# Kernel tuning notes

Measured on AMD Instinct MI355X. Metric: run time of the kernel, lower is better.

The kernel has to match this reference:

```python
import jax, jax.numpy as jnp
from jax import lax
import numpy as np

L = 8            # NMF rank (n_components)
NMF_ITERS = 50   # fixed multiplicative-update iterations
EPS = 1.1920929e-07  # float32 machine eps, as sklearn uses


def nmf_mu(V, key):
    """Multiplicative-update NMF (Frobenius loss), sklearn-style random init.
    V: [T, M] nonnegative. Returns W:[T,L], H:[L,M]."""
    T, M = V.shape
    kW, kH = jax.random.split(key)
    avg = jnp.sqrt(jnp.mean(V) / L)
    W0 = avg * jax.random.uniform(kW, (T, L), dtype=V.dtype)
    H0 = avg * jax.random.uniform(kH, (L, M), dtype=V.dtype)

    def step(carry, _):
        W, H = carry
        # H update: H *= (W^T V) / (W^T W H)
        H = H * (W.T @ V) / (W.T @ W @ H + EPS)
        # W update: W *= (V H^T) / (W H H^T)
        W = W * (V @ H.T) / (W @ (H @ H.T) + EPS)
        return (W, H), None

    (W, H), _ = lax.scan(step, (W0, H0), None, length=NMF_ITERS)
    return W, H


def pointwise_conv(w, x):
    # 1x1x1 Conv3d == channel mix: w [C_out, C_in], x [n, C_in, D, H, W]
    return jnp.einsum('oc,ncdhw->nodhw', w, x)


def setup_inputs() -> dict:
    key = jax.random.key(0)
    k0, k1, k2, k3, k4 = jax.random.split(key, 5)
    C = 64
    eps = jax.random.normal(k0, (1, C, 16, 64, 64), dtype=jnp.float32)
    s = 1.0 / np.sqrt(C)  # keep pre-activation variance ~1 (like torch init scale)
    w_pre = jax.random.normal(k1, (C, C), dtype=jnp.float32) * s
    b_pre = jax.random.normal(k2, (C,), dtype=jnp.float32) * s
    w_post1 = jax.random.normal(k3, (C, C), dtype=jnp.float32) * s
    w_post2 = jax.random.normal(k4, (C, C), dtype=jnp.float32) * s
    return {"eps": eps, "w_pre": w_pre, "b_pre": b_pre,
            "w_post1": w_post1, "w_post2": w_post2}


def reference(eps, w_pre, b_pre, w_post1, w_post2):
    n, t, k, a, b = eps.shape
    # xi_pre: 1x1x1 conv + bias + ReLU (ReLU guarantees nonnegative NMF input)
    Vst = jax.nn.relu(pointwise_conv(w_pre, eps) + b_pre[None, :, None, None, None])
    V = Vst.reshape(t, k * a * b)  # n == 1
    W, H = nmf_mu(V, jax.random.key(0))
    Vst_hat = (W @ H).reshape(n, t, k, a, b)
    error = jnp.linalg.norm(Vst - Vst_hat)  # torch.dist (Frobenius)
    # xi_post: conv(no bias) -> ReLU -> conv(no bias)
    y = jax.nn.relu(pointwise_conv(w_post1, Vst_hat))
    eps_hat = pointwise_conv(w_post2, y)
    return eps_hat, error
```

## Files before the change

kernel.cpp:

```cpp
#include <hip/hip_runtime.h>
#include <stdint.h>

#define JAX_PARTITIONABLE 1

constexpr int kC = 64;
constexpr int kS = 65536;
constexpr int kL = 8;
constexpr int kIters = 50;
constexpr int kBlocks = 256;
constexpr int kThreads = 512;
constexpr int kCols = 256;
constexpr int kGroups = 16;
constexpr int kEntries = 576;
constexpr float kEps = 1.1920929e-07f;

#define AGENT __HIP_MEMORY_SCOPE_AGENT

struct Ctl {
  unsigned root;  unsigned pad0[31];
  unsigned leaf[16][32];
  float mean_sum; float err_sum; float pad1[30];
  float B[3][kGroups][kEntries];
};

__device__ __forceinline__ uint2 tf2x32(unsigned k0, unsigned k1,
                                        unsigned x0, unsigned x1) {
  unsigned k2 = k0 ^ k1 ^ 0x1BD11BDAu;
  x0 += k0; x1 += k1;
#define TF_RND(r) { x0 += x1; x1 = (x1 << (r)) | (x1 >> (32 - (r))); x1 ^= x0; }
  TF_RND(13) TF_RND(15) TF_RND(26) TF_RND(6)
  x0 += k1; x1 += k2 + 1u;
  TF_RND(17) TF_RND(29) TF_RND(16) TF_RND(24)
  x0 += k2; x1 += k0 + 2u;
  TF_RND(13) TF_RND(15) TF_RND(26) TF_RND(6)
  x0 += k0; x1 += k1 + 3u;
  TF_RND(17) TF_RND(29) TF_RND(16) TF_RND(24)
  x0 += k1; x1 += k2 + 4u;
  TF_RND(13) TF_RND(15) TF_RND(26) TF_RND(6)
  x0 += k2; x1 += k0 + 5u;
#undef TF_RND
  return make_uint2(x0, x1);
}

__device__ __forceinline__ float u01(unsigned b) {
  return __uint_as_float((b >> 9) | 0x3f800000u) - 1.0f;
}

__device__ __forceinline__ void gridbar(Ctl* ctl, unsigned& round) {
  ++round;
  __syncthreads();
  if (threadIdx.x == 0) {
    const unsigned target = round * 16u;
    const unsigned leaf = blockIdx.x & 15u;
    unsigned a = __hip_atomic_fetch_add(&ctl->leaf[leaf][0], 1u,
                                        __ATOMIC_RELAXED, AGENT);
    if (a == target - 1u)
      __hip_atomic_fetch_add(&ctl->root, 1u, __ATOMIC_RELAXED, AGENT);
    while (__hip_atomic_load(&ctl->root, __ATOMIC_RELAXED, AGENT) < target)
      __builtin_amdgcn_s_sleep(1);
    __builtin_amdgcn_fence(__ATOMIC_ACQUIRE, "agent");
  }
  __syncthreads();
}

__global__ void init_ctl(unsigned* ws) {
  const unsigned n = (unsigned)(sizeof(Ctl) / 4);
  for (unsigned i = blockIdx.x * blockDim.x + threadIdx.x; i < n;
       i += gridDim.x * blockDim.x)
    ws[i] = 0u;
}

__global__ __launch_bounds__(kThreads, 2) void fsam_nmf(
    const float* __restrict__ eps, const float* __restrict__ w_pre,
    const float* __restrict__ b_pre, const float* __restrict__ w_post1,
    const float* __restrict__ w_post2, float* __restrict__ out, Ctl* ctl) {
  __shared__ __align__(16) float Vs[kC][260];
  __shared__ __align__(16) float Hs[kL][260];
  __shared__ __align__(16) float Pn[kL][260];
  __shared__ __align__(16) float Pv[4][512];
  __shared__ __align__(16) float Ph[16][64];
  __shared__ __align__(16) float Ws[kC][kL];
  __shared__ __align__(16) float WtWs[kL * kL];
  __shared__ __align__(16) float hhts[kL * kL];
  __shared__ float reds[8];

  const int tid = threadIdx.x;
  const int t = tid & 255;
  const int q = tid >> 8;
  const int obase = q * 32;
  const int s = blockIdx.x * kCols + t;
  unsigned bar_round = 0;

  float acc[32];
#pragma unroll
  for (int o = 0; o < 32; ++o) acc[o] = b_pre[obase + o];
  for (int c = 0; c < kC; ++c) {
    const float e = eps[c * kS + s];
#pragma unroll
    for (int o = 0; o < 32; ++o)
      acc[o] = fmaf(w_pre[(obase + o) * kC + c], e, acc[o]);
  }
  float lsum = 0.0f;
#pragma unroll
  for (int o = 0; o < 32; ++o) {
    acc[o] = fmaxf(acc[o], 0.0f);
    Vs[obase + o][t] = acc[o];
    lsum += acc[o];
  }
  {
    float r = lsum;
#pragma unroll
    for (int off = 32; off > 0; off >>= 1) r += __shfl_down(r, off, 64);
    if ((tid & 63) == 0) reds[tid >> 6] = r;
    __syncthreads();
    if (tid == 0) {
      float sm = 0.0f;
#pragma unroll
      for (int w = 0; w < 8; ++w) sm += reds[w];
      __hip_atomic_fetch_add(&ctl->mean_sum, sm, __ATOMIC_RELAXED, AGENT);
    }
  }
  gridbar(ctl, bar_round);
  const float avg = sqrtf(
      __hip_atomic_load(&ctl->mean_sum, __ATOMIC_RELAXED, AGENT) *
      (1.0f / (4194304.0f * 8.0f)));

#if JAX_PARTITIONABLE
  const uint2 kw = tf2x32(0u, 0u, 0u, 0u);
  const uint2 kh = tf2x32(0u, 0u, 0u, 1u);
#else
  const uint2 A0 = tf2x32(0u, 0u, 0u, 2u);
  const uint2 A1 = tf2x32(0u, 0u, 1u, 3u);
  const uint2 kw = make_uint2(A0.x, A1.x);
  const uint2 kh = make_uint2(A0.y, A1.y);
#endif

  float h[kL] = {0, 0, 0, 0, 0, 0, 0, 0};
  if (q == 0) {
#if JAX_PARTITIONABLE
#pragma unroll
    for (int l = 0; l < kL; ++l) {
      uint2 r = tf2x32(kh.x, kh.y, 0u, (unsigned)(l * kS + s));
      h[l] = avg * u01(r.x ^ r.y);
    }
#else
#pragma unroll
    for (int l = 0; l < 4; ++l) {
      unsigned i = (unsigned)(l * kS + s);
      uint2 r = tf2x32(kh.x, kh.y, i, i + 262144u);
      h[l] = avg * u01(r.x);
      h[l + 4] = avg * u01(r.y);
    }
#endif
  }
  {
#if JAX_PARTITIONABLE
    uint2 r0 = tf2x32(kw.x, kw.y, 0u, (unsigned)tid);
    (&Ws[0][0])[tid] = avg * u01(r0.x ^ r0.y);
#else
    if (tid < 256) {
      uint2 r = tf2x32(kw.x, kw.y, (unsigned)tid, (unsigned)(tid + 256));
      (&Ws[0][0])[tid] = avg * u01(r.x);
      (&Ws[0][0])[tid + 256] = avg * u01(r.y);
    }
#endif
  }
  __syncthreads();
  if (tid < kL * kL) {
    const int l = tid >> 3, j = tid & 7;
    float sum = 0.0f;
    for (int c = 0; c < kC; ++c) sum = fmaf(Ws[c][l], Ws[c][j], sum);
    WtWs[tid] = sum;
  }
  __syncthreads();

  for (int it = 0; it < kIters; ++it) {
    float num[kL] = {0, 0, 0, 0, 0, 0, 0, 0};
    for (int ci = 0; ci < 32; ++ci) {
      const int c = obase + ci;
      const float v = Vs[c][t];
      const float4 w0 = *(const float4*)&Ws[c][0];
      const float4 w1 = *(const float4*)&Ws[c][4];
      num[0] = fmaf(v, w0.x, num[0]); num[1] = fmaf(v, w0.y, num[1]);
      num[2] = fmaf(v, w0.z, num[2]); num[3] = fmaf(v, w0.w, num[3]);
      num[4] = fmaf(v, w1.x, num[4]); num[5] = fmaf(v, w1.y, num[5]);
      num[6] = fmaf(v, w1.z, num[6]); num[7] = fmaf(v, w1.w, num[7]);
    }
    if (q == 1) {
#pragma unroll
      for (int l = 0; l < kL; ++l) Pn[l][t] = num[l];
    }
    __syncthreads();
    if (q == 0) {
      float hn[kL];
#pragma unroll
      for (int l = 0; l < kL; ++l) {
        const float4 a = *(const float4*)&WtWs[l * kL];
        const float4 b = *(const float4*)&WtWs[l * kL + 4];
        float d = kEps;
        d = fmaf(a.x, h[0], d); d = fmaf(a.y, h[1], d);
        d = fmaf(a.z, h[2], d); d = fmaf(a.w, h[3], d);
        d = fmaf(b.x, h[4], d); d = fmaf(b.y, h[5], d);
        d = fmaf(b.z, h[6], d); d = fmaf(b.w, h[7], d);
        hn[l] = h[l] * (num[l] + Pn[l][t]) / d;
      }
#pragma unroll
      for (int l = 0; l < kL; ++l) { h[l] = hn[l]; Hs[l][t] = hn[l]; }
    } else if ((blockIdx.x >> 4) == 1) {
      float* nb = &ctl->B[(it + 1) % 3][blockIdx.x & 15][0];
      for (int k = t; k < kEntries; k += 256)
        __hip_atomic_store(&nb[k], 0.0f, __ATOMIC_RELAXED, AGENT);
    }
    __syncthreads();

    {
      const int range = tid >> 7;
      const int tile = tid & 127;
      const int c0 = (tile >> 2) * 2;
      const int l0 = (tile & 3) * 2;
      const int sbeg = range * 64;
      float a00 = 0, a01 = 0, a10 = 0, a11 = 0;
      for (int s4 = sbeg; s4 < sbeg + 64; s4 += 4) {
        const float4 h0 = *(const float4*)&Hs[l0][s4];
        const float4 h1 = *(const float4*)&Hs[l0 + 1][s4];
        const float4 v0 = *(const float4*)&Vs[c0][s4];
        const float4 v1 = *(const float4*)&Vs[c0 + 1][s4];
        a00 = fmaf(v0.x, h0.x, a00); a00 = fmaf(v0.y, h0.y, a00);
        a00 = fmaf(v0.z, h0.z, a00); a00 = fmaf(v0.w, h0.w, a00);
        a01 = fmaf(v0.x, h1.x, a01); a01 = fmaf(v0.y, h1.y, a01);
        a01 = fmaf(v0.z, h1.z, a01); a01 = fmaf(v0.w, h1.w, a01);
        a10 = fmaf(v1.x, h0.x, a10); a10 = fmaf(v1.y, h0.y, a10);
        a10 = fmaf(v1.z, h0.z, a10); a10 = fmaf(v1.w, h0.w, a10);
        a11 = fmaf(v1.x, h1.x, a11); a11 = fmaf(v1.y, h1.y, a11);
        a11 = fmaf(v1.z, h1.z, a11); a11 = fmaf(v1.w, h1.w, a11);
      }
      Pv[range][c0 * 8 + l0] = a00;
      Pv[range][c0 * 8 + l0 + 1] = a01;
      Pv[range][(c0 + 1) * 8 + l0] = a10;
      Pv[range][(c0 + 1) * 8 + l0 + 1] = a11;
    }
    if (tid < 256) {
      const int tile = tid >> 4, range = tid & 15;
      const int j0 = (tile >> 2) * 2, l0 = (tile & 3) * 2;
      const int sbeg = range * 16;
      float a00 = 0, a01 = 0, a10 = 0, a11 = 0;
      for (int s4 = sbeg; s4 < sbeg + 16; s4 += 4) {
        const float4 x0 = *(const float4*)&Hs[j0][s4];
        const float4 x1 = *(const float4*)&Hs[j0 + 1][s4];
        const float4 y0 = *(const float4*)&Hs[l0][s4];
        const float4 y1 = *(const float4*)&Hs[l0 + 1][s4];
        a00 = fmaf(x0.x, y0.x, a00); a00 = fmaf(x0.y, y0.y, a00);
        a00 = fmaf(x0.z, y0.z, a00); a00 = fmaf(x0.w, y0.w, a00);
        a01 = fmaf(x0.x, y1.x, a01); a01 = fmaf(x0.y, y1.y, a01);
        a01 = fmaf(x0.z, y1.z, a01); a01 = fmaf(x0.w, y1.w, a01);
        a10 = fmaf(x1.x, y0.x, a10); a10 = fmaf(x1.y, y0.y, a10);
        a10 = fmaf(x1.z, y0.z, a10); a10 = fmaf(x1.w, y0.w, a10);
        a11 = fmaf(x1.x, y1.x, a11); a11 = fmaf(x1.y, y1.y, a11);
        a11 = fmaf(x1.z, y1.z, a11); a11 = fmaf(x1.w, y1.w, a11);
      }
      Ph[range][j0 * 8 + l0] = a00;
      Ph[range][j0 * 8 + l0 + 1] = a01;
      Ph[range][(j0 + 1) * 8 + l0] = a10;
      Ph[range][(j0 + 1) * 8 + l0 + 1] = a11;
    }
    __syncthreads();

    float* Bg = &ctl->B[it % 3][blockIdx.x & 15][0];
    {
      const float v = Pv[0][tid & 511] + Pv[1][tid & 511] +
                      Pv[2][tid & 511] + Pv[3][tid & 511];
      __hip_atomic_fetch_add(&Bg[tid], v, __ATOMIC_RELAXED, AGENT);
    }
    if (tid >= 448) {
      const int e = tid - 448;
      float v = 0.0f;
#pragma unroll
      for (int r = 0; r < 16; ++r) v += Ph[r][e];
      __hip_atomic_fetch_add(&Bg[512 + e], v, __ATOMIC_RELAXED, AGENT);
    }

    gridbar(ctl, bar_round);

    const float* Bb = &ctl->B[it % 3][0][0];
    float v = 0.0f;
    {
#pragma unroll
      for (int g = 0; g < kGroups; ++g) v += Bb[g * kEntries + tid];
    }
    if (tid < kL * kL) {
      float sum = 0.0f;
#pragma unroll
      for (int g = 0; g < kGroups; ++g) sum += Bb[g * kEntries + 512 + tid];
      hhts[tid] = sum;
    }
    __syncthreads();
    float wn;
    {
      const int c0 = tid >> 3, l0 = tid & 7;
      float d = kEps;
#pragma unroll
      for (int j = 0; j < kL; ++j) d = fmaf(Ws[c0][j], hhts[j * kL + l0], d);
      wn = (&Ws[0][0])[tid] * v / d;
    }
    __syncthreads();
    (&Ws[0][0])[tid] = wn;
    __syncthreads();
    if (tid < kL * kL) {
      const int l = tid >> 3, j = tid & 7;
      float sum = 0.0f;
      for (int c = 0; c < kC; ++c) sum = fmaf(Ws[c][l], Ws[c][j], sum);
      WtWs[tid] = sum;
    }
    __syncthreads();
  }

  if (q == 1) {
#pragma unroll
    for (int l = 0; l < kL; ++l) h[l] = Hs[l][t];
  }
  float errp = 0.0f;
  for (int ci = 0; ci < 32; ++ci) {
    const int c = obase + ci;
    const float4 w0 = *(const float4*)&Ws[c][0];
    const float4 w1 = *(const float4*)&Ws[c][4];
    float tcc = 0.0f;
    tcc = fmaf(w0.x, h[0], tcc); tcc = fmaf(w0.y, h[1], tcc);
    tcc = fmaf(w0.z, h[2], tcc); tcc = fmaf(w0.w, h[3], tcc);
    tcc = fmaf(w1.x, h[4], tcc); tcc = fmaf(w1.y, h[5], tcc);
    tcc = fmaf(w1.z, h[6], tcc); tcc = fmaf(w1.w, h[7], tcc);
    const float d = Vs[c][t] - tcc;
    errp = fmaf(d, d, errp);
    Vs[c][t] = tcc;
  }
  {
    float r = errp;
#pragma unroll
    for (int off = 32; off > 0; off >>= 1) r += __shfl_down(r, off, 64);
    __syncthreads();
    if ((tid & 63) == 0) reds[tid >> 6] = r;
    __syncthreads();
    if (tid == 0) {
      float sm = 0.0f;
#pragma unroll
      for (int w = 0; w < 8; ++w) sm += reds[w];
      __hip_atomic_fetch_add(&ctl->err_sum, sm, __ATOMIC_RELAXED, AGENT);
    }
  }
  __syncthreads();
  float yacc[32];
#pragma unroll
  for (int o = 0; o < 32; ++o) yacc[o] = 0.0f;
  for (int c = 0; c < kC; ++c) {
    const float vv = Vs[c][t];
#pragma unroll
    for (int o = 0; o < 32; ++o)
      yacc[o] = fmaf(w_post1[(obase + o) * kC + c], vv, yacc[o]);
  }
  __syncthreads();
#pragma unroll
  for (int o = 0; o < 32; ++o) Vs[obase + o][t] = fmaxf(yacc[o], 0.0f);
  __syncthreads();
  float outacc[32];
#pragma unroll
  for (int o = 0; o < 32; ++o) outacc[o] = 0.0f;
  for (int c = 0; c < kC; ++c) {
    const float yv = Vs[c][t];
#pragma unroll
    for (int o = 0; o < 32; ++o)
      outacc[o] = fmaf(w_post2[(obase + o) * kC + c], yv, outacc[o]);
  }
#pragma unroll
  for (int o = 0; o < 32; ++o) out[(obase + o) * kS + s] = outacc[o];

  gridbar(ctl, bar_round);
  if (blockIdx.x == 0 && tid == 0)
    out[kC * kS] = sqrtf(__hip_atomic_load(&ctl->err_sum, __ATOMIC_RELAXED, AGENT));
}

extern "C" void kernel_launch(void* const* d_in, const int* in_sizes, int n_in,
                              void* d_out, int out_size, void* d_ws, size_t ws_size,
                              hipStream_t stream) {
  (void)in_sizes; (void)n_in; (void)out_size; (void)ws_size;
  const float* eps     = (const float*)d_in[0];
  const float* w_pre   = (const float*)d_in[1];
  const float* b_pre   = (const float*)d_in[2];
  const float* w_post1 = (const float*)d_in[3];
  const float* w_post2 = (const float*)d_in[4];
  float* out = (float*)d_out;
  Ctl* ctl = (Ctl*)d_ws;

  init_ctl<<<64, 256, 0, stream>>>((unsigned*)d_ws);
  fsam_nmf<<<kBlocks, kThreads, 0, stream>>>(eps, w_pre, b_pre, w_post1,
                                             w_post2, out, ctl);
}
```

Measured before the change: 741.3 us.

## Split NMF grid into 512 blocks of 128 columns with four channel quarters

Doubles the persistent grid to 512 blocks, each owning 128 spatial columns, and splits channels across four 128-thread groups instead of two 256-thread groups. H is kept in shared memory, and the per-iteration numerator partials are reduced across three Pn buffers. The two-level grid barrier is widened to 32 leaves, and launch bounds now target four blocks per CU. The aim is to raise occupancy and cut per-block serial work per iteration, at the cost of more blocks contending at each of the roughly fifty grid barriers and a smaller register budget per thread.

```diff
diff --git a/kernel.cpp b/kernel.cpp
--- a/kernel.cpp
+++ b/kernel.cpp
@@ -7,18 +7,19 @@
 constexpr int kS = 65536;
 constexpr int kL = 8;
 constexpr int kIters = 50;
-constexpr int kBlocks = 256;
+constexpr int kBlocks = 512;
 constexpr int kThreads = 512;
-constexpr int kCols = 256;
+constexpr int kCols = 128;
 constexpr int kGroups = 16;
 constexpr int kEntries = 576;
+constexpr int kPitch = 132;
 constexpr float kEps = 1.1920929e-07f;
 
 #define AGENT __HIP_MEMORY_SCOPE_AGENT
 
 struct Ctl {
   unsigned root;  unsigned pad0[31];
-  unsigned leaf[16][32];
+  unsigned leaf[32][32];
   float mean_sum; float err_sum; float pad1[30];
   float B[3][kGroups][kEntries];
 };
@@ -50,12 +51,12 @@
   ++round;
   __syncthreads();
   if (threadIdx.x == 0) {
-    const unsigned target = round * 16u;
-    const unsigned leaf = blockIdx.x & 15u;
+    const unsigned leaf = blockIdx.x & 31u;
     unsigned a = __hip_atomic_fetch_add(&ctl->leaf[leaf][0], 1u,
                                         __ATOMIC_RELAXED, AGENT);
-    if (a == target - 1u)
+    if (a == round * 16u - 1u)
       __hip_atomic_fetch_add(&ctl->root, 1u, __ATOMIC_RELAXED, AGENT);
+    const unsigned target = round * 32u;
     while (__hip_atomic_load(&ctl->root, __ATOMIC_RELAXED, AGENT) < target)
       __builtin_amdgcn_s_sleep(1);
     __builtin_amdgcn_fence(__ATOMIC_ACQUIRE, "agent");
@@ -70,13 +71,13 @@
     ws[i] = 0u;
 }
 
-__global__ __launch_bounds__(kThreads, 2) void fsam_nmf(
+__global__ __launch_bounds__(kThreads, 4) void fsam_nmf(
     const float* __restrict__ eps, const float* __restrict__ w_pre,
     const float* __restrict__ b_pre, const float* __restrict__ w_post1,
     const float* __restrict__ w_post2, float* __restrict__ out, Ctl* ctl) {
-  __shared__ __align__(16) float Vs[kC][260];
-  __shared__ __align__(16) float Hs[kL][260];
-  __shared__ __align__(16) float Pn[kL][260];
+  __shared__ __align__(16) float Vs[kC][kPitch];
+  __shared__ __align__(16) float Hs[kL][kPitch];
+  __shared__ __align__(16) float Pn[3][kL][kPitch];
   __shared__ __align__(16) float Pv[4][512];
   __shared__ __align__(16) float Ph[16][64];
   __shared__ __align__(16) float Ws[kC][kL];
@@ -85,24 +86,24 @@
   __shared__ float reds[8];
 
   const int tid = threadIdx.x;
-  const int t = tid & 255;
-  const int q = tid >> 8;
-  const int obase = q * 32;
+  const int t = tid & 127;
+  const int q = tid >> 7;
+  const int obase = q * 16;
   const int s = blockIdx.x * kCols + t;
   unsigned bar_round = 0;
 
-  float acc[32];
-#pragma unroll
-  for (int o = 0; o < 32; ++o) acc[o] = b_pre[obase + o];
+  float acc[16];
+#pragma unroll
+  for (int o = 0; o < 16; ++o) acc[o] = b_pre[obase + o];
   for (int c = 0; c < kC; ++c) {
     const float e = eps[c * kS + s];
 #pragma unroll
-    for (int o = 0; o < 32; ++o)
+    for (int o = 0; o < 16; ++o)
       acc[o] = fmaf(w_pre[(obase + o) * kC + c], e, acc[o]);
   }
   float lsum = 0.0f;
 #pragma unroll
-  for (int o = 0; o < 32; ++o) {
+  for (int o = 0; o < 16; ++o) {
     acc[o] = fmaxf(acc[o], 0.0f);
     Vs[obase + o][t] = acc[o];
     lsum += acc[o];
@@ -135,21 +136,20 @@
   const uint2 kh = make_uint2(A0.y, A1.y);
 #endif
 
-  float h[kL] = {0, 0, 0, 0, 0, 0, 0, 0};
   if (q == 0) {
 #if JAX_PARTITIONABLE
 #pragma unroll
     for (int l = 0; l < kL; ++l) {
       uint2 r = tf2x32(kh.x, kh.y, 0u, (unsigned)(l * kS + s));
-      h[l] = avg * u01(r.x ^ r.y);
+      Hs[l][t] = avg * u01(r.x ^ r.y);
     }
 #else
 #pragma unroll
     for (int l = 0; l < 4; ++l) {
       unsigned i = (unsigned)(l * kS + s);
       uint2 r = tf2x32(kh.x, kh.y, i, i + 262144u);
-      h[l] = avg * u01(r.x);
-      h[l + 4] = avg * u01(r.y);
+      Hs[l][t] = avg * u01(r.x);
+      Hs[l + 4][t] = avg * u01(r.y);
     }
 #endif
   }
@@ -176,7 +176,7 @@
 
   for (int it = 0; it < kIters; ++it) {
     float num[kL] = {0, 0, 0, 0, 0, 0, 0, 0};
-    for (int ci = 0; ci < 32; ++ci) {
+    for (int ci = 0; ci < 16; ++ci) {
       const int c = obase + ci;
       const float v = Vs[c][t];
       const float4 w0 = *(const float4*)&Ws[c][0];
@@ -186,13 +186,15 @@
       num[4] = fmaf(v, w1.x, num[4]); num[5] = fmaf(v, w1.y, num[5]);
       num[6] = fmaf(v, w1.z, num[6]); num[7] = fmaf(v, w1.w, num[7]);
     }
-    if (q == 1) {
-#pragma unroll
-      for (int l = 0; l < kL; ++l) Pn[l][t] = num[l];
+    if (q != 0) {
+#pragma unroll
+      for (int l = 0; l < kL; ++l) Pn[q - 1][l][t] = num[l];
     }
     __syncthreads();
     if (q == 0) {
-      float hn[kL];
+      float h[kL], hn[kL];
+#pragma unroll
+      for (int l = 0; l < kL; ++l) h[l] = Hs[l][t];
 #pragma unroll
       for (int l = 0; l < kL; ++l) {
         const float4 a = *(const float4*)&WtWs[l * kL];
@@ -202,13 +204,14 @@
         d = fmaf(a.z, h[2], d); d = fmaf(a.w, h[3], d);
         d = fmaf(b.x, h[4], d); d = fmaf(b.y, h[5], d);
         d = fmaf(b.z, h[6], d); d = fmaf(b.w, h[7], d);
-        hn[l] = h[l] * (num[l] + Pn[l][t]) / d;
+        const float nm = num[l] + Pn[0][l][t] + Pn[1][l][t] + Pn[2][l][t];
+        hn[l] = h[l] * nm / d;
       }
 #pragma unroll
-      for (int l = 0; l < kL; ++l) { h[l] = hn[l]; Hs[l][t] = hn[l]; }
+      for (int l = 0; l < kL; ++l) Hs[l][t] = hn[l];
     } else if ((blockIdx.x >> 4) == 1) {
       float* nb = &ctl->B[(it + 1) % 3][blockIdx.x & 15][0];
-      for (int k = t; k < kEntries; k += 256)
+      for (int k = tid - 128; k < kEntries; k += 384)
         __hip_atomic_store(&nb[k], 0.0f, __ATOMIC_RELAXED, AGENT);
     }
     __syncthreads();
@@ -218,9 +221,9 @@
       const int tile = tid & 127;
       const int c0 = (tile >> 2) * 2;
       const int l0 = (tile & 3) * 2;
-      const int sbeg = range * 64;
+      const int sbeg = range * 32;
       float a00 = 0, a01 = 0, a10 = 0, a11 = 0;
-      for (int s4 = sbeg; s4 < sbeg + 64; s4 += 4) {
+      for (int s4 = sbeg; s4 < sbeg + 32; s4 += 4) {
         const float4 h0 = *(const float4*)&Hs[l0][s4];
         const float4 h1 = *(const float4*)&Hs[l0 + 1][s4];
         const float4 v0 = *(const float4*)&Vs[c0][s4];
@@ -242,9 +245,9 @@
     if (tid < 256) {
       const int tile = tid >> 4, range = tid & 15;
       const int j0 = (tile >> 2) * 2, l0 = (tile & 3) * 2;
-      const int sbeg = range * 16;
+      const int sbeg = range * 8;
       float a00 = 0, a01 = 0, a10 = 0, a11 = 0;
-      for (int s4 = sbeg; s4 < sbeg + 16; s4 += 4) {
+      for (int s4 = sbeg; s4 < sbeg + 8; s4 += 4) {
         const float4 x0 = *(const float4*)&Hs[j0][s4];
         const float4 x1 = *(const float4*)&Hs[j0 + 1][s4];
         const float4 y0 = *(const float4*)&Hs[l0][s4];
@@ -267,8 +270,7 @@
 
     float* Bg = &ctl->B[it % 3][blockIdx.x & 15][0];
     {
-      const float v = Pv[0][tid & 511] + Pv[1][tid & 511] +
-                      Pv[2][tid & 511] + Pv[3][tid & 511];
+      const float v = Pv[0][tid] + Pv[1][tid] + Pv[2][tid] + Pv[3][tid];
       __hip_atomic_fetch_add(&Bg[tid], v, __ATOMIC_RELAXED, AGENT);
     }
     if (tid >= 448) {
@@ -314,12 +316,11 @@
     __syncthreads();
   }
 
-  if (q == 1) {
-#pragma unroll
-    for (int l = 0; l < kL; ++l) h[l] = Hs[l][t];
-  }
+  float h[kL];
+#pragma unroll
+  for (int l = 0; l < kL; ++l) h[l] = Hs[l][t];
   float errp = 0.0f;
-  for (int ci = 0; ci < 32; ++ci) {
+  for (int ci = 0; ci < 16; ++ci) {
     const int c = obase + ci;
     const float4 w0 = *(const float4*)&Ws[c][0];
     const float4 w1 = *(const float4*)&Ws[c][4];
@@ -347,30 +348,30 @@
     }
   }
   __syncthreads();
-  float yacc[32];
-#pragma unroll
-  for (int o = 0; o < 32; ++o) yacc[o] = 0.0f;
+  float yacc[16];
+#pragma unroll
+  for (int o = 0; o < 16; ++o) yacc[o] = 0.0f;
   for (int c = 0; c < kC; ++c) {
     const float vv = Vs[c][t];
 #pragma unroll
-    for (int o = 0; o < 32; ++o)
+    for (int o = 0; o < 16; ++o)
       yacc[o] = fmaf(w_post1[(obase + o) * kC + c], vv, yacc[o]);
   }
   __syncthreads();
 #pragma unroll
-  for (int o = 0; o < 32; ++o) Vs[obase + o][t] = fmaxf(yacc[o], 0.0f);
-  __syncthreads();
-  float outacc[32];
-#pragma unroll
-  for (int o = 0; o < 32; ++o) outacc[o] = 0.0f;
+  for (int o = 0; o < 16; ++o) Vs[obase + o][t] = fmaxf(yacc[o], 0.0f);
+  __syncthreads();
+  float outacc[16];
+#pragma unroll
+  for (int o = 0; o < 16; ++o) outacc[o] = 0.0f;
   for (int c = 0; c < kC; ++c) {
     const float yv = Vs[c][t];
 #pragma unroll
-    for (int o = 0; o < 32; ++o)
+    for (int o = 0; o < 16; ++o)
       outacc[o] = fmaf(w_post2[(obase + o) * kC + c], yv, outacc[o]);
   }
 #pragma unroll
-  for (int o = 0; o < 32; ++o) out[(obase + o) * kS + s] = outacc[o];
+  for (int o = 0; o < 16; ++o) out[(obase + o) * kS + s] = outacc[o];
 
   gridbar(ctl, bar_round);
   if (blockIdx.x == 0 && tid == 0)
```

After: 952.4 us. 1.28x slower.
